# Optimization experiments

Measured on AMD Instinct MI355X. Metric: run time of the kernel, lower is better.

Reference implementation:

```python
import jax, jax.numpy as jnp
import numpy as np

B, D, T, K = 16, 256, 1024, 8192
BETA = 0.25
EPS = 1e-10


def setup_inputs() -> dict:
    key = jax.random.key(0)
    k1, k2 = jax.random.split(key)
    z = jax.random.normal(k1, (B, D, T), dtype=jnp.float32)
    # codebook initialized uniform(-1/K, 1/K) like the torch module
    embedding = jax.random.uniform(k2, (K, D), dtype=jnp.float32,
                                   minval=-1.0 / K, maxval=1.0 / K)
    return {"z": z, "embedding": embedding}


def reference(z, embedding):
    # z: [B, D, T] -> [B, T, D]
    zf = jnp.transpose(z, (0, 2, 1))
    # squared L2 distances to each codebook entry: [B, T, K]
    d = (jnp.sum(zf ** 2, axis=2, keepdims=True)
         + jnp.sum(embedding ** 2, axis=1)
         - 2.0 * jnp.einsum('btd,kd->btk', zf, embedding))
    idx = jnp.argmin(d, axis=2)                         # [B, T] int
    min_encodings = jax.nn.one_hot(idx, K, dtype=jnp.float32)  # [B, T, K]
    z_q = embedding[idx]                                # [B, T, D]
    z_q = jnp.transpose(z_q, (0, 2, 1))                 # [B, D, T]

    codebook_loss = jnp.mean((z - jax.lax.stop_gradient(z_q)) ** 2)
    commitment_loss = jnp.mean((jax.lax.stop_gradient(z) - z_q) ** 2)
    vq_loss = codebook_loss + BETA * commitment_loss

    # perplexity exactly as in torch code: mean over dim 0 only -> [T, K]
    avg_probs = jnp.mean(min_encodings, axis=0)
    perplexity = jnp.exp(-jnp.sum(avg_probs * jnp.log(avg_probs + EPS)))

    return z_q, vq_loss, perplexity, idx
```

## Files before the change

kernel.cpp:

```cpp
#include <hip/hip_runtime.h>
#include <hip/hip_bf16.h>
#include <float.h>
#include <math.h>

#define NB 16
#define ND 256
#define NT 1024
#define NK 8192
#define NBT (NB*NT)
#define PTS 64
#define KCH 512
#define DBLK 32
#define NSTAGE ((NK/KCH)*(ND/DBLK))



__global__ void k_prep(const float* __restrict__ emb, float* __restrict__ ssq,
                       double* __restrict__ loss_sum, double* __restrict__ ent_sum) {
    int k = blockIdx.x * 4 + (threadIdx.x >> 6);
    int lane = threadIdx.x & 63;
    float4 v = *reinterpret_cast<const float4*>(emb + (size_t)k * ND + lane * 4);
    float s = v.x * v.x + v.y * v.y + v.z * v.z + v.w * v.w;
#pragma unroll
    for (int off = 32; off; off >>= 1) s += __shfl_down(s, off, 64);
    if (lane == 0) ssq[k] = s;
    if (blockIdx.x == 0 && threadIdx.x == 0) { *loss_sum = 0.0; *ent_sum = 0.0; }
}

__device__ __forceinline__ int es_col(int dd, int kk) {
    return kk ^ (((dd >> 2) & 7) << 2) ^ (((kk >> 5) & 1) << 2);
}

__global__ __launch_bounds__(512)
void k_main(const float* __restrict__ z, const float* __restrict__ emb,
            const float* __restrict__ ssq, int* __restrict__ idx_out,
            float* __restrict__ zq_out, float* __restrict__ idxf_out,
            double* __restrict__ loss_sum) {
    __shared__ float Zs[ND][PTS];
    __shared__ float As[PTS];
    __shared__ int   bkS[PTS];
    __shared__ double wred[8];
    __shared__ __align__(16) char ubuf[ND * (PTS + 1) * 4];
    float* EsF  = reinterpret_cast<float*>(ubuf);
    float* redD = reinterpret_cast<float*>(ubuf);
    int*   redK = reinterpret_cast<int*>(ubuf + PTS * 65 * 4);
    float (*Qs)[PTS + 1] = reinterpret_cast<float (*)[PTS + 1]>(ubuf);

    const int tid = threadIdx.x;
    const int bid = blockIdx.x;
    const int b  = bid >> 4;
    const int t0 = (bid & 15) * PTS;
    const float* zb = z + ((size_t)b * ND) * NT + t0;

#pragma unroll
    for (int it = 0; it < 8; ++it) {
        int i4 = (it * 512 + tid) * 4;
        int d = i4 >> 6, i = i4 & 63;
        *reinterpret_cast<float4*>(&Zs[d][i]) =
            *reinterpret_cast<const float4*>(zb + (size_t)d * NT + i);
    }
    __syncthreads();

    if (tid < PTS) {
        float a = 0.f;
        for (int d = 0; d < ND; ++d) {
            float x = Zs[d][tid];
            a = __fadd_rn(a, __fmul_rn(x, x));
        }
        As[tid] = a;
    }

    const int py  = tid >> 6;
    const int kx  = tid & 63;
    const int skk = tid >> 3;
    const int sd4 = (tid & 7) * 4;

    float best[8]; int bk[8];
#pragma unroll
    for (int p = 0; p < 8; ++p) { best[p] = FLT_MAX; bk[p] = 0; }

    float4 creg[8];
#pragma unroll
    for (int it = 0; it < 8; ++it)
        creg[it] = *reinterpret_cast<const float4*>(emb + (size_t)(it * 64 + skk) * ND + sd4);

    int stage = 0;
    for (int kc = 0; kc < NK / KCH; ++kc) {
        float acc[8][8];
#pragma unroll
        for (int p = 0; p < 8; ++p)
#pragma unroll
            for (int q = 0; q < 8; ++q) acc[p][q] = 0.f;

        for (int db = 0; db < ND / DBLK; ++db, ++stage) {
            __syncthreads();
#pragma unroll
            for (int it = 0; it < 8; ++it) {
                int kk = it * 64 + skk;
                const float* vp = reinterpret_cast<const float*>(&creg[it]);
#pragma unroll
                for (int j = 0; j < 4; ++j) {
                    int dd = sd4 + j;
                    EsF[dd * KCH + es_col(dd, kk)] = vp[j];
                }
            }
            float4 nreg[8];
            bool have_next = (stage + 1 < NSTAGE);
            if (have_next) {
                int ns = stage + 1;
                int nkc = ns >> 3, ndb = ns & 7;
                const float* ebase = emb + (size_t)nkc * KCH * ND + ndb * DBLK;
#pragma unroll
                for (int it = 0; it < 8; ++it)
                    nreg[it] = *reinterpret_cast<const float4*>(
                        ebase + (size_t)(it * 64 + skk) * ND + sd4);
            }
            __syncthreads();

            const int zd0 = db * DBLK;
#pragma unroll 4
            for (int dd = 0; dd < DBLK; ++dd) {
                int c0 = es_col(dd, kx * 8);
                int c1 = es_col(dd, kx * 8 + 4);
                float4 e0 = *reinterpret_cast<const float4*>(&EsF[dd * KCH + c0]);
                float4 e1 = *reinterpret_cast<const float4*>(&EsF[dd * KCH + c1]);
                float4 za0 = *reinterpret_cast<const float4*>(&Zs[zd0 + dd][py * 8]);
                float4 za1 = *reinterpret_cast<const float4*>(&Zs[zd0 + dd][py * 8 + 4]);
                float zr[8] = {za0.x, za0.y, za0.z, za0.w, za1.x, za1.y, za1.z, za1.w};
                float er[8] = {e0.x, e0.y, e0.z, e0.w, e1.x, e1.y, e1.z, e1.w};
#pragma unroll
                for (int p = 0; p < 8; ++p)
#pragma unroll
                    for (int q = 0; q < 8; ++q)
                        acc[p][q] = fmaf(zr[p], er[q], acc[p][q]);
            }
            if (have_next) {
#pragma unroll
                for (int it = 0; it < 8; ++it) creg[it] = nreg[it];
            }
        }
        const float* sq = ssq + kc * KCH + kx * 8;
        float4 s0 = *reinterpret_cast<const float4*>(sq);
        float4 s1 = *reinterpret_cast<const float4*>(sq + 4);
        float sqv[8] = {s0.x, s0.y, s0.z, s0.w, s1.x, s1.y, s1.z, s1.w};
#pragma unroll
        for (int p = 0; p < 8; ++p) {
            float A = As[py * 8 + p];
#pragma unroll
            for (int q = 0; q < 8; ++q) {
                float s = __fadd_rn(A, sqv[q]);
                float dist = __fsub_rn(s, 2.0f * acc[p][q]);
                if (dist < best[p]) { best[p] = dist; bk[p] = kc * KCH + kx * 8 + q; }
            }
        }
    }
    __syncthreads();
#pragma unroll
    for (int p = 0; p < 8; ++p) {
        redD[(py * 8 + p) * 65 + kx] = best[p];
        redK[(py * 8 + p) * 65 + kx] = bk[p];
    }
    __syncthreads();
    if (tid < PTS) {
        float bd = redD[tid * 65]; int bb = redK[tid * 65];
        for (int x = 1; x < 64; ++x) {
            float dx = redD[tid * 65 + x]; int kk2 = redK[tid * 65 + x];
            if (dx < bd || (dx == bd && kk2 < bb)) { bd = dx; bb = kk2; }
        }
        bkS[tid] = bb;
        int pg = b * NT + t0 + tid;
        idx_out[pg] = bb;
        idxf_out[pg] = (float)bb;
    }
    __syncthreads();

#pragma unroll
    for (int it = 0; it < 32; ++it) {
        int e = it * 512 + tid;
        int d = e & 255, pt = e >> 8;
        Qs[d][pt] = emb[(size_t)bkS[pt] * ND + d];
    }
    __syncthreads();

    {
        const int pt = tid & 63, dq = tid >> 6;
        double ls = 0.0;
        for (int j = 0; j < 32; ++j) {
            int d = dq * 32 + j;
            float qv = Qs[d][pt];
            float diff = __fsub_rn(Zs[d][pt], qv);
            ls = fma((double)diff, (double)diff, ls);
            zq_out[((size_t)(b * ND + d)) * NT + t0 + pt] = qv;
        }
#pragma unroll
        for (int off = 32; off; off >>= 1) ls += __shfl_down(ls, off, 64);
        if ((tid & 63) == 0) wred[tid >> 6] = ls;
    }
    __syncthreads();
    if (tid == 0) {
        double tot = 0.0;
#pragma unroll
        for (int w = 0; w < 8; ++w) tot += wred[w];
        atomicAdd(loss_sum, tot);
    }
}

__global__ void k_ent(const int* __restrict__ idx, double* __restrict__ ent_sum) {
    __shared__ double wred[4];
    int t = blockIdx.x * 256 + threadIdx.x;
    int v[16];
#pragma unroll
    for (int i = 0; i < NB; ++i) v[i] = idx[i * NT + t];
    double s = 0.0;
#pragma unroll
    for (int i = 0; i < NB; ++i) {
        bool first = true;
        for (int j = 0; j < i; ++j) if (v[j] == v[i]) first = false;
        if (first) {
            int c = 1;
            for (int j = i + 1; j < NB; ++j) c += (v[j] == v[i]);
            float p = (float)c * 0.0625f;
            s += (double)(p * logf(p + 1e-10f));
        }
    }
#pragma unroll
    for (int off = 32; off; off >>= 1) s += __shfl_down(s, off, 64);
    if ((threadIdx.x & 63) == 0) wred[threadIdx.x >> 6] = s;
    __syncthreads();
    if (threadIdx.x == 0) {
        double tot = wred[0] + wred[1] + wred[2] + wred[3];
        atomicAdd(ent_sum, tot);
    }
}

__global__ void k_fin(const double* __restrict__ loss_sum,
                      const double* __restrict__ ent_sum, float* __restrict__ out) {
    if (threadIdx.x == 0 && blockIdx.x == 0) {
        float L = (float)(*loss_sum / (double)(NB * ND * NT));
        out[4194304] = __fadd_rn(L, 0.25f * L);
        float S = (float)(-*ent_sum);
        out[4194305] = expf(fminf(S, 87.0f));
    }
}

extern "C" void kernel_launch(void* const* d_in, const int* in_sizes, int n_in,
                              void* d_out, int out_size, void* d_ws, size_t ws_size,
                              hipStream_t stream) {
    const float* z   = (const float*)d_in[0];
    const float* emb = (const float*)d_in[1];
    float* out = (float*)d_out;

    float*  ssq      = (float*)d_ws;
    int*    idx      = (int*)((char*)d_ws + 32768);
    double* loss_sum = (double*)((char*)d_ws + 98304);
    double* ent_sum  = (double*)((char*)d_ws + 98312);

    float* zq   = out;
    float* idxf = out + 4194306;

    k_prep<<<NK / 4, 256, 0, stream>>>(emb, ssq, loss_sum, ent_sum);
    k_main<<<NBT / PTS, 512, 0, stream>>>(z, emb, ssq, idx, zq, idxf, loss_sum);
    k_ent<<<NT / 256, 256, 0, stream>>>(idx, ent_sum);
    k_fin<<<1, 64, 0, stream>>>(loss_sum, ent_sum, out);
}
```

Baseline: 817.0 us.

## Double-buffer codebook tiles in LDS with one barrier per stage

Measured after the change: 1.758 ms. 2.15x slower.

```diff
diff --git a/kernel.cpp b/kernel.cpp
--- a/kernel.cpp
+++ b/kernel.cpp
@@ -10,7 +10,9 @@
 #define NBT (NB*NT)
 #define PTS 64
 #define KCH 512
-#define DBLK 32
+#define DBLK 16
+#define ESTRIDE 516
+#define ESBUF (DBLK*ESTRIDE)
 #define NSTAGE ((NK/KCH)*(ND/DBLK))
 
 
@@ -27,8 +29,8 @@
     if (blockIdx.x == 0 && threadIdx.x == 0) { *loss_sum = 0.0; *ent_sum = 0.0; }
 }
 
-__device__ __forceinline__ int es_col(int dd, int kk) {
-    return kk ^ (((dd >> 2) & 7) << 2) ^ (((kk >> 5) & 1) << 2);
+__device__ __forceinline__ int es_col(int kk) {
+    return kk ^ (((kk >> 5) & 7) << 2);
 }
 
 __global__ __launch_bounds__(512)
@@ -70,21 +72,35 @@
         As[tid] = a;
     }
 
-    const int py  = tid >> 6;
-    const int kx  = tid & 63;
-    const int skk = tid >> 3;
-    const int sd4 = (tid & 7) * 4;
+    const int py = tid >> 6;
+    const int kx = tid & 63;
+    const int colw = es_col(tid);
+    const int col0 = es_col(kx * 8);
+    const int col1 = col0 ^ 4;
 
     float best[8]; int bk[8];
 #pragma unroll
     for (int p = 0; p < 8; ++p) { best[p] = FLT_MAX; bk[p] = 0; }
 
-    float4 creg[8];
-#pragma unroll
-    for (int it = 0; it < 8; ++it)
-        creg[it] = *reinterpret_cast<const float4*>(emb + (size_t)(it * 64 + skk) * ND + sd4);
-
-    int stage = 0;
+    const float* erow0 = emb + (size_t)tid * ND;
+    float4 creg[4];
+#pragma unroll
+    for (int j = 0; j < 4; ++j)
+        creg[j] = *reinterpret_cast<const float4*>(erow0 + j * 4);
+    {
+        float* w = EsF + colw;
+#pragma unroll
+        for (int j = 0; j < 4; ++j) {
+            const float* v = reinterpret_cast<const float*>(&creg[j]);
+#pragma unroll
+            for (int i = 0; i < 4; ++i) w[(j * 4 + i) * ESTRIDE] = v[i];
+        }
+    }
+#pragma unroll
+    for (int j = 0; j < 4; ++j)
+        creg[j] = *reinterpret_cast<const float4*>(erow0 + DBLK + j * 4);
+    __syncthreads();
+
     for (int kc = 0; kc < NK / KCH; ++kc) {
         float acc[8][8];
 #pragma unroll
@@ -92,40 +108,35 @@
 #pragma unroll
             for (int q = 0; q < 8; ++q) acc[p][q] = 0.f;
 
-        for (int db = 0; db < ND / DBLK; ++db, ++stage) {
-            __syncthreads();
-#pragma unroll
-            for (int it = 0; it < 8; ++it) {
-                int kk = it * 64 + skk;
-                const float* vp = reinterpret_cast<const float*>(&creg[it]);
+        for (int db = 0; db < ND / DBLK; ++db) {
+            const int s = kc * (ND / DBLK) + db;
+            const int cur = s & 1;
+            if (s + 1 < NSTAGE) {
+                float* w = EsF + (cur ^ 1) * ESBUF + colw;
 #pragma unroll
                 for (int j = 0; j < 4; ++j) {
-                    int dd = sd4 + j;
-                    EsF[dd * KCH + es_col(dd, kk)] = vp[j];
+                    const float* v = reinterpret_cast<const float*>(&creg[j]);
+#pragma unroll
+                    for (int i = 0; i < 4; ++i) w[(j * 4 + i) * ESTRIDE] = v[i];
+                }
+                if (s + 2 < NSTAGE) {
+                    const int ns = s + 2;
+                    const float* p2 = emb + (size_t)((ns >> 4) * KCH + tid) * ND
+                                          + (ns & 15) * DBLK;
+#pragma unroll
+                    for (int j = 0; j < 4; ++j)
+                        creg[j] = *reinterpret_cast<const float4*>(p2 + j * 4);
                 }
             }
-            float4 nreg[8];
-            bool have_next = (stage + 1 < NSTAGE);
-            if (have_next) {
-                int ns = stage + 1;
-                int nkc = ns >> 3, ndb = ns & 7;
-                const float* ebase = emb + (size_t)nkc * KCH * ND + ndb * DBLK;
-#pragma unroll
-                for (int it = 0; it < 8; ++it)
-                    nreg[it] = *reinterpret_cast<const float4*>(
-                        ebase + (size_t)(it * 64 + skk) * ND + sd4);
-            }
-            __syncthreads();
-
-            const int zd0 = db * DBLK;
-#pragma unroll 4
+            const float* e0b = EsF + cur * ESBUF + col0;
+            const float* e1b = EsF + cur * ESBUF + col1;
+            const float* zrow = &Zs[db * DBLK][py * 8];
+#pragma unroll
             for (int dd = 0; dd < DBLK; ++dd) {
-                int c0 = es_col(dd, kx * 8);
-                int c1 = es_col(dd, kx * 8 + 4);
-                float4 e0 = *reinterpret_cast<const float4*>(&EsF[dd * KCH + c0]);
-                float4 e1 = *reinterpret_cast<const float4*>(&EsF[dd * KCH + c1]);
-                float4 za0 = *reinterpret_cast<const float4*>(&Zs[zd0 + dd][py * 8]);
-                float4 za1 = *reinterpret_cast<const float4*>(&Zs[zd0 + dd][py * 8 + 4]);
+                float4 e0  = *reinterpret_cast<const float4*>(e0b + dd * ESTRIDE);
+                float4 e1  = *reinterpret_cast<const float4*>(e1b + dd * ESTRIDE);
+                float4 za0 = *reinterpret_cast<const float4*>(zrow + dd * PTS);
+                float4 za1 = *reinterpret_cast<const float4*>(zrow + dd * PTS + 4);
                 float zr[8] = {za0.x, za0.y, za0.z, za0.w, za1.x, za1.y, za1.z, za1.w};
                 float er[8] = {e0.x, e0.y, e0.z, e0.w, e1.x, e1.y, e1.z, e1.w};
 #pragma unroll
@@ -134,10 +145,7 @@
                     for (int q = 0; q < 8; ++q)
                         acc[p][q] = fmaf(zr[p], er[q], acc[p][q]);
             }
-            if (have_next) {
-#pragma unroll
-                for (int it = 0; it < 8; ++it) creg[it] = nreg[it];
-            }
+            __syncthreads();
         }
         const float* sq = ssq + kc * KCH + kx * 8;
         float4 s0 = *reinterpret_cast<const float4*>(sq);
```
